# Kernel optimization log

Hardware: AMD Instinct MI355X
Metric: run time of the kernel (lower is better)

Reference implementation:

```python
import jax, jax.numpy as jnp
import numpy as np

B, H, L, D = 4, 16, 2048, 64
TOPK = 128


def setup_inputs() -> dict:
    key = jax.random.key(0)
    k1, k2, k3 = jax.random.split(key, 3)
    Q = jax.random.normal(k1, (B, H, L, D), dtype=jnp.float32)
    K = jax.random.normal(k2, (B, H, L, D), dtype=jnp.float32)
    V = jax.random.normal(k3, (B, H, L, D), dtype=jnp.float32)
    return {"Q": Q, "K": K, "V": V, "topk": TOPK}


def reference(Q, K, V, topk):
    # activation = softmax(d**-0.5 * x), as the docstring prescribes for vanilla attention
    scale = Q.shape[-1] ** -0.5
    neg = -jnp.finfo(Q.dtype).max  # max_neg_value, matching torch
    b, h, lq, d = Q.shape
    lk = K.shape[-2]

    # dots: [B,H,Lq,Lk]
    dots = jnp.einsum('bhqd,bhkd->bhqk', Q, K)
    # causal masking (True entries masked)
    causal = jnp.triu(jnp.ones((lq, lk), dtype=bool), 1)
    dots = jnp.where(causal, neg, dots)

    # top-k sparsification along keys
    top_dots, top_inds = jax.lax.top_k(dots, topk)          # [B,H,Lq,k]
    top_attn = jax.nn.softmax(top_dots * scale, axis=-1)    # activation on top values only

    # scatter activated values back into a zeroed [B,H,Lq,Lk] attention matrix
    bi = jnp.arange(b)[:, None, None, None]
    hi = jnp.arange(h)[None, :, None, None]
    qi = jnp.arange(lq)[None, None, :, None]
    attn = jnp.zeros_like(dots).at[bi, hi, qi, top_inds].set(top_attn)

    # out = attn @ V : [B,H,Lq,Dv]
    return jnp.einsum('bhqk,bhkd->bhqd', attn, V)
```

## Files before the change

kernel.cpp:

```cpp
#include <hip/hip_runtime.h>
#include <float.h>
#include <stdint.h>

#define QB        8
#define NTHREADS  512
#define LQ        2048
#define NDIM      64
#define KSEL      128
#define CHK       512
#define SSTR      516
#define LDS_BYTES 28800
#define WS_NEEDED (2u * 8388608u * 2u)

typedef __attribute__((ext_vector_type(8))) short  s8v;
typedef __attribute__((ext_vector_type(4))) float  f32x4;

__device__ __forceinline__ unsigned ordf(float f) {
  unsigned u = __float_as_uint(f);
  return (u & 0x80000000u) ? ~u : (u | 0x80000000u);
}
__device__ __forceinline__ float unordf(unsigned u) {
  unsigned x = (u & 0x80000000u) ? (u & 0x7FFFFFFFu) : ~u;
  return __uint_as_float(x);
}
__device__ __forceinline__ unsigned short f2bf(float f) {
  unsigned u = __float_as_uint(f);
  return (unsigned short)((u + 0x7FFFu + ((u >> 16) & 1u)) >> 16);
}
__device__ __forceinline__ float bf2f(unsigned short h) {
  return __uint_as_float(((unsigned)h) << 16);
}

extern "C" __global__ void __launch_bounds__(256)
convert_k(const float4* __restrict__ K4, ushort4* __restrict__ Khi,
          ushort4* __restrict__ Klo) {
  const int idx = blockIdx.x * 256 + threadIdx.x;
  const float4 f = K4[idx];
  ushort4 h, l;
  h.x = f2bf(f.x); l.x = f2bf(f.x - bf2f(h.x));
  h.y = f2bf(f.y); l.y = f2bf(f.y - bf2f(h.y));
  h.z = f2bf(f.z); l.z = f2bf(f.z - bf2f(h.z));
  h.w = f2bf(f.w); l.w = f2bf(f.w - bf2f(h.w));
  Khi[idx] = h;
  Klo[idx] = l;
}

__device__ __forceinline__ void select_pv(
    uint4 U0, uint4 U1, uint4 U2, uint4 U3,
    uint4 U4, uint4 U5, uint4 U6, uint4 U7,
    const int g8, const int lane,
    int* __restrict__ list, float* __restrict__ wl,
    const float* __restrict__ Vg, float* __restrict__ outp) {
  const float C = 0.18033688011112042f;
  const unsigned long long ltmask = (1ull << lane) - 1ull;

  unsigned p = 0;
  int k = KSEL;
  bool exact = false;
#pragma unroll 1
  for (int b = 31; b >= 0; --b) {
    const unsigned T = p | (1u << b);
    int cnt = 0;
#define CNT_G(i, Uv) \
    if (i <= g8) { \
      cnt += (int)__popcll(__ballot(Uv.x >= T)); \
      cnt += (int)__popcll(__ballot(Uv.y >= T)); \
      cnt += (int)__popcll(__ballot(Uv.z >= T)); \
      cnt += (int)__popcll(__ballot(Uv.w >= T)); \
    }
    CNT_G(0, U0) CNT_G(1, U1) CNT_G(2, U2) CNT_G(3, U3)
    CNT_G(4, U4) CNT_G(5, U5) CNT_G(6, U6) CNT_G(7, U7)
#undef CNT_G
    if (cnt >= KSEL) {
      p = T;
      if (cnt == KSEL) { exact = true; break; }
    } else {
      k = KSEL - cnt;
    }
  }
  const unsigned tu   = exact ? (p - 1u) : p;
  const int      krem = exact ? 0 : k;
  const float    wt   = exact ? 0.f : exp2f(unordf(p) * C);

  float zacc = 0.f;
  int base = 0;
#define COLL_C(i, uexpr, cidx) { \
    const unsigned ui = (uexpr); \
    const unsigned long long bm = __ballot(ui > tu); \
    if (ui > tu) { \
      const int pos = base + (int)__popcll(bm & ltmask); \
      const float wv = exp2f(unordf(ui) * C); \
      list[pos] = (i << 8) + (lane << 2) + cidx; \
      wl[pos]   = wv; \
      zacc += wv; \
    } \
    base += (int)__popcll(bm); }
#define COLL_G(i, Uv) \
    if (i <= g8) { COLL_C(i, Uv.x, 0) COLL_C(i, Uv.y, 1) COLL_C(i, Uv.z, 2) COLL_C(i, Uv.w, 3) }
  COLL_G(0, U0) COLL_G(1, U1) COLL_G(2, U2) COLL_G(3, U3)
  COLL_G(4, U4) COLL_G(5, U5) COLL_G(6, U6) COLL_G(7, U7)
#undef COLL_G
#undef COLL_C

  int n = base;
  if (wt > 0.f && krem > 0) {
    int carry = 0;
#define TIE_G(i, Uv) \
    if (i <= g8 && carry < krem) { \
      const bool e0 = (Uv.x == tu), e1 = (Uv.y == tu), e2 = (Uv.z == tu), e3 = (Uv.w == tu); \
      const unsigned long long b0 = __ballot(e0), b1 = __ballot(e1); \
      const unsigned long long b2 = __ballot(e2), b3 = __ballot(e3); \
      int r = carry + (int)__popcll(b0 & ltmask) + (int)__popcll(b1 & ltmask) + \
              (int)__popcll(b2 & ltmask) + (int)__popcll(b3 & ltmask); \
      const int jb = (i << 8) + (lane << 2); \
      if (e0) { if (r < krem) { list[base + r] = jb + 0; wl[base + r] = wt; zacc += wt; } ++r; } \
      if (e1) { if (r < krem) { list[base + r] = jb + 1; wl[base + r] = wt; zacc += wt; } ++r; } \
      if (e2) { if (r < krem) { list[base + r] = jb + 2; wl[base + r] = wt; zacc += wt; } ++r; } \
      if (e3) { if (r < krem) { list[base + r] = jb + 3; wl[base + r] = wt; zacc += wt; } ++r; } \
      carry += (int)__popcll(b0) + (int)__popcll(b1) + \
               (int)__popcll(b2) + (int)__popcll(b3); \
    }
    TIE_G(0, U0) TIE_G(1, U1) TIE_G(2, U2) TIE_G(3, U3)
    TIE_G(4, U4) TIE_G(5, U5) TIE_G(6, U6) TIE_G(7, U7)
#undef TIE_G
    n = base + krem;
  }
  float Z = zacc;
#pragma unroll
  for (int off = 1; off < 64; off <<= 1) Z += __shfl_xor(Z, off, 64);
  __threadfence_block();

  const int grp = lane >> 4;
  const int dl4 = (lane & 15) << 2;
  float4 acc4 = {0.f, 0.f, 0.f, 0.f};
  int i = 0;
  for (; i + 8 <= n; i += 8) {
    const int   ja = list[i + grp];
    const int   jb = list[i + 4 + grp];
    const float wa = wl[i + grp];
    const float wb = wl[i + 4 + grp];
    const float4 va = *(const float4*)&Vg[(size_t)ja * NDIM + dl4];
    const float4 vb = *(const float4*)&Vg[(size_t)jb * NDIM + dl4];
    acc4.x += wa * va.x + wb * vb.x;
    acc4.y += wa * va.y + wb * vb.y;
    acc4.z += wa * va.z + wb * vb.z;
    acc4.w += wa * va.w + wb * vb.w;
  }
  for (; i < n; i += 4) {
    const bool  ok = (i + grp) < n;
    const int   j  = ok ? list[i + grp] : 0;
    const float w  = ok ? wl[i + grp]   : 0.f;
    const float4 v = *(const float4*)&Vg[(size_t)j * NDIM + dl4];
    acc4.x += w * v.x;
    acc4.y += w * v.y;
    acc4.z += w * v.z;
    acc4.w += w * v.w;
  }
  acc4.x += __shfl_xor(acc4.x, 16, 64);
  acc4.y += __shfl_xor(acc4.y, 16, 64);
  acc4.z += __shfl_xor(acc4.z, 16, 64);
  acc4.w += __shfl_xor(acc4.w, 16, 64);
  acc4.x += __shfl_xor(acc4.x, 32, 64);
  acc4.y += __shfl_xor(acc4.y, 32, 64);
  acc4.z += __shfl_xor(acc4.z, 32, 64);
  acc4.w += __shfl_xor(acc4.w, 32, 64);
  if (grp == 0) {
    const float rz = 1.f / Z;
    float4 o;
    o.x = acc4.x * rz;
    o.y = acc4.y * rz;
    o.z = acc4.z * rz;
    o.w = acc4.w * rz;
    *(float4*)(outp + dl4) = o;
  }
}

extern "C" __global__ void __launch_bounds__(NTHREADS, 4)
topk_attn_mfma(const float* __restrict__ Qg_, const float* __restrict__ Vg_,
               const unsigned short* __restrict__ Khi_,
               const unsigned short* __restrict__ Klo_,
               float* __restrict__ Out) {
  extern __shared__ char lds[];
  float*          s_chunk = (float*)(lds);
  unsigned short* qs_hi   = (unsigned short*)(lds + 16512);
  unsigned short* qs_lo   = (unsigned short*)(lds + 18560);
  int*            lists   = (int*)(lds + 20608);
  float*          wlist   = (float*)(lds + 24704);

  const int id  = blockIdx.x;
  const int xcd = id & 7;
  const int k   = id >> 3;
  const int bh  = xcd + ((k >> 8) << 3);
  const int qb  = k & 255;

  const int q0   = qb * QB;
  const int tid  = threadIdx.x;
  const int lane = tid & 63;
  const int wid  = tid >> 6;
  const int m16  = lane & 15;
  const int quad = lane >> 4;

  const float* Qg  = Qg_ + ((size_t)(bh * LQ + q0)) * NDIM;
  const float* Vg  = Vg_ + ((size_t)bh) * LQ * NDIM;
  const unsigned short* Khi = Khi_ + ((size_t)bh) * LQ * NDIM;
  const unsigned short* Klo = Klo_ + ((size_t)bh) * LQ * NDIM;

#pragma unroll
  for (int e = tid; e < 16 * NDIM; e += NTHREADS) {
    const int r = e >> 6;
    const float f = (r < QB) ? Qg[e] : 0.f;
    const unsigned short hh = f2bf(f);
    qs_hi[e] = hh;
    qs_lo[e] = f2bf(f - bf2f(hh));
  }
  __syncthreads();

  const unsigned short* qh = qs_hi + m16 * NDIM + quad * 8;
  const unsigned short* ql = qs_lo + m16 * NDIM + quad * 8;
  const s8v Ah0 = *(const s8v*)qh;
  const s8v Ah1 = *(const s8v*)(qh + 32);
  const s8v Al0 = *(const s8v*)ql;
  const s8v Al1 = *(const s8v*)(ql + 32);

  const int q    = q0 + wid;
  const int g8   = q >> 8;
  const int qmax = q0 + QB - 1;
  const int nt   = (qmax >> 4) + 1;
  const int nch  = (qmax >> 9) + 1;

  auto produce = [&](const int ch) {
#pragma unroll 1
    for (int t = 0; t < 4; ++t) {
      const int jt = (ch << 5) + wid + (t << 3);
      if (jt >= nt) continue;
      const int jc  = (jt << 4) + m16;
      const int jcl = jc - (ch << 9);
      const unsigned short* kh = Khi + (size_t)jc * NDIM + quad * 8;
      const unsigned short* kl = Klo + (size_t)jc * NDIM + quad * 8;
      const s8v Bh0 = *(const s8v*)kh;
      const s8v Bh1 = *(const s8v*)(kh + 32);
      const s8v Bl0 = *(const s8v*)kl;
      const s8v Bl1 = *(const s8v*)(kl + 32);
      f32x4 c = {0.f, 0.f, 0.f, 0.f};
      c = __builtin_amdgcn_mfma_f32_16x16x32_bf16(Ah0, Bh0, c, 0, 0, 0);
      c = __builtin_amdgcn_mfma_f32_16x16x32_bf16(Al0, Bh0, c, 0, 0, 0);
      c = __builtin_amdgcn_mfma_f32_16x16x32_bf16(Ah1, Bh1, c, 0, 0, 0);
      c = __builtin_amdgcn_mfma_f32_16x16x32_bf16(Al1, Bh1, c, 0, 0, 0);
      c = __builtin_amdgcn_mfma_f32_16x16x32_bf16(Ah0, Bl0, c, 0, 0, 0);
      c = __builtin_amdgcn_mfma_f32_16x16x32_bf16(Ah1, Bl1, c, 0, 0, 0);
      if (quad < 2) {
#pragma unroll
        for (int reg = 0; reg < 4; ++reg) {
          const int r = quad * 4 + reg;
          s_chunk[r * SSTR + jcl] = c[reg];
        }
      }
    }
  };

  uint4 U0 = make_uint4(0,0,0,0), U1 = make_uint4(0,0,0,0);
  uint4 U2 = make_uint4(0,0,0,0), U3 = make_uint4(0,0,0,0);
  uint4 U4 = make_uint4(0,0,0,0), U5 = make_uint4(0,0,0,0);
  uint4 U6 = make_uint4(0,0,0,0), U7 = make_uint4(0,0,0,0);

  const float4* row4 = (const float4*)(s_chunk + wid * SSTR);
#define CONSUME_HALF(i8, Uv) \
    if (i8 <= g8) { \
      const float4 a = row4[((i8 & 1) << 6) + lane]; \
      const int jb = (i8 << 8) + (lane << 2); \
      Uv.x = (jb + 0 <= q) ? ordf(a.x) : 0u; \
      Uv.y = (jb + 1 <= q) ? ordf(a.y) : 0u; \
      Uv.z = (jb + 2 <= q) ? ordf(a.z) : 0u; \
      Uv.w = (jb + 3 <= q) ? ordf(a.w) : 0u; \
    }

  produce(0);
  __syncthreads();
  CONSUME_HALF(0, U0)
  CONSUME_HALF(1, U1)
  if (nch > 1) {
    __syncthreads();
    produce(1);
    __syncthreads();
    CONSUME_HALF(2, U2)
    CONSUME_HALF(3, U3)
    if (nch > 2) {
      __syncthreads();
      produce(2);
      __syncthreads();
      CONSUME_HALF(4, U4)
      CONSUME_HALF(5, U5)
      if (nch > 3) {
        __syncthreads();
        produce(3);
        __syncthreads();
        CONSUME_HALF(6, U6)
        CONSUME_HALF(7, U7)
      }
    }
  }
#undef CONSUME_HALF

  select_pv(U0, U1, U2, U3, U4, U5, U6, U7, g8, lane,
            lists + wid * KSEL, wlist + wid * KSEL, Vg,
            Out + ((size_t)(bh * LQ + q)) * NDIM);
}

#define FB_QB        8
#define FB_LDS_BYTES 73760

extern "C" __global__ void __launch_bounds__(NTHREADS, 4)
topk_attn_fb(const float* __restrict__ Qg_, const float* __restrict__ Kg_,
             const float* __restrict__ Vg_, float* __restrict__ Out) {
  extern __shared__ char lds[];
  float* s_phys = (float*)(lds);
  int*   lists  = (int*)(lds + 65536);
  float* wlist  = (float*)(lds + 69632);
  float* qs     = (float*)(lds + 65536);

  const int id  = blockIdx.x;
  const int xcd = id & 7;
  const int w   = id >> 3;
  const int bh  = w >> 5;
  const int qb  = ((w & 31) << 3) + xcd;

  const int q0   = qb * FB_QB;
  const int tid  = threadIdx.x;
  const int lane = tid & 63;
  const int wid  = tid >> 6;

  const float* Qg = Qg_ + ((size_t)(bh * LQ + q0)) * NDIM;
  const float* Kg = Kg_ + ((size_t)bh) * LQ * NDIM;
  const float* Vg = Vg_ + ((size_t)bh) * LQ * NDIM;

  if (tid < FB_QB * NDIM / 4) ((float4*)qs)[tid] = ((const float4*)Qg)[tid];
  __syncthreads();

  const int tq   = tid >> 8;
  const int tk   = tid & 255;
  const int j0   = tk << 3;
  const int qmax = q0 + FB_QB - 1;
  const bool active = (j0 <= qmax);

  float acc[4][8];
#pragma unroll
  for (int i = 0; i < 4; ++i)
#pragma unroll
    for (int j = 0; j < 8; ++j) acc[i][j] = 0.f;

  if (active) {
    const float4* K4  = (const float4*)(Kg + (size_t)j0 * NDIM);
    const float4* qs4 = (const float4*)(qs + tq * 4 * NDIM);
#pragma unroll 1
    for (int d4 = 0; d4 < 16; ++d4) {
      float4 qv[4];
#pragma unroll
      for (int i = 0; i < 4; ++i) qv[i] = qs4[i * 16 + d4];
#pragma unroll
      for (int g = 0; g < 4; ++g) {
        const float4 k0 = K4[(2 * g + 0) * 16 + d4];
        const float4 k1 = K4[(2 * g + 1) * 16 + d4];
#pragma unroll
        for (int i = 0; i < 4; ++i) {
          acc[i][2 * g + 0] += qv[i].x * k0.x + qv[i].y * k0.y +
                               qv[i].z * k0.z + qv[i].w * k0.w;
          acc[i][2 * g + 1] += qv[i].x * k1.x + qv[i].y * k1.y +
                               qv[i].z * k1.z + qv[i].w * k1.w;
        }
      }
    }
  }
  __syncthreads();

#pragma unroll
  for (int i = 0; i < 4; ++i) {
    const int q = q0 + tq * 4 + i;
    float4* srow4 = (float4*)(s_phys + (tq * 4 + i) * LQ);
    float4 lo, hi;
    lo.x = (j0 + 0 <= q) ? acc[i][0] : -FLT_MAX;
    lo.y = (j0 + 1 <= q) ? acc[i][1] : -FLT_MAX;
    lo.z = (j0 + 2 <= q) ? acc[i][2] : -FLT_MAX;
    lo.w = (j0 + 3 <= q) ? acc[i][3] : -FLT_MAX;
    hi.x = (j0 + 4 <= q) ? acc[i][4] : -FLT_MAX;
    hi.y = (j0 + 5 <= q) ? acc[i][5] : -FLT_MAX;
    hi.z = (j0 + 6 <= q) ? acc[i][6] : -FLT_MAX;
    hi.w = (j0 + 7 <= q) ? acc[i][7] : -FLT_MAX;
    srow4[tk * 2 + 0] = lo;
    srow4[tk * 2 + 1] = hi;
  }
  __syncthreads();

  const float C = 0.18033688011112042f;
  const int qi = wid;
  const int q = q0 + qi;
  const float* srow = s_phys + qi * LQ;
  const float4* srow4 = (const float4*)srow;

  unsigned u[32];
#pragma unroll
  for (int i = 0; i < 8; ++i) {
    const float4 v = srow4[lane + (i << 6)];
    u[4 * i + 0] = ordf(v.x);
    u[4 * i + 1] = ordf(v.y);
    u[4 * i + 2] = ordf(v.z);
    u[4 * i + 3] = ordf(v.w);
  }

  unsigned p = 0;
  int k = KSEL;
#pragma unroll 1
  for (int b = 31; b >= 0; --b) {
    const unsigned T = p | (1u << b);
    int cnt = 0;
#pragma unroll
    for (int i = 0; i < 32; ++i)
      cnt += (int)__popcll(__ballot(u[i] >= T));
    if (cnt >= KSEL) p = T;
    else             k = KSEL - cnt;
  }
  const unsigned tu = p;
  const int krem = k;
  const float wt = exp2f(unordf(tu) * C);

  const unsigned long long ltmask = (1ull << lane) - 1ull;
  float zacc = 0.f;
  int myeq = 0;
  int base = 0;
#pragma unroll
  for (int i = 0; i < 32; ++i) {
    const unsigned ui = u[i];
    const unsigned long long b = __ballot(ui > tu);
    if (ui > tu) {
      const int pos = base + (int)__popcll(b & ltmask);
      const int j = ((i >> 2) << 8) + (lane << 2) + (i & 3);
      const float wv = exp2f(unordf(ui) * C);
      lists[qi * KSEL + pos] = j;
      wlist[qi * KSEL + pos] = wv;
      zacc += wv;
    }
    base += (int)__popcll(b);
    myeq += (ui == tu) ? 1 : 0;
  }
  int n = base;
  if (wt > 0.f) {
    int te = myeq;
#pragma unroll
    for (int off = 1; off < 64; off <<= 1) te += __shfl_xor(te, off, 64);
    if (te == krem) {
#pragma unroll
      for (int i = 0; i < 32; ++i) {
        const unsigned long long b = __ballot(u[i] == tu);
        if (u[i] == tu) {
          const int pos = base + (int)__popcll(b & ltmask);
          const int j = ((i >> 2) << 8) + (lane << 2) + (i & 3);
          lists[qi * KSEL + pos] = j;
          wlist[qi * KSEL + pos] = wt;
          zacc += wt;
        }
        base += (int)__popcll(b);
      }
      n = base;
    } else {
      if (lane == 0) {
        int taken = 0, pos = base;
        for (int j = 0; j < LQ && taken < krem; ++j) {
          if (ordf(srow[j]) == tu) {
            lists[qi * KSEL + pos] = j;
            wlist[qi * KSEL + pos] = wt;
            pos++; taken++;
          }
        }
        zacc += wt * (float)krem;
      }
      n = KSEL;
    }
  }
  float Z = zacc;
#pragma unroll
  for (int off = 1; off < 64; off <<= 1) Z += __shfl_xor(Z, off, 64);
  __threadfence_block();

  float accv = 0.f;
  int i = 0;
  for (; i + 8 <= n; i += 8) {
    const int4   ja = *(const int4*)  &lists[qi * KSEL + i];
    const int4   jb = *(const int4*)  &lists[qi * KSEL + i + 4];
    const float4 wa = *(const float4*)&wlist[qi * KSEL + i];
    const float4 wb = *(const float4*)&wlist[qi * KSEL + i + 4];
    const float v0 = Vg[(size_t)ja.x * NDIM + lane];
    const float v1 = Vg[(size_t)ja.y * NDIM + lane];
    const float v2 = Vg[(size_t)ja.z * NDIM + lane];
    const float v3 = Vg[(size_t)ja.w * NDIM + lane];
    const float v4 = Vg[(size_t)jb.x * NDIM + lane];
    const float v5 = Vg[(size_t)jb.y * NDIM + lane];
    const float v6 = Vg[(size_t)jb.z * NDIM + lane];
    const float v7 = Vg[(size_t)jb.w * NDIM + lane];
    accv += wa.x * v0 + wa.y * v1 + wa.z * v2 + wa.w * v3 +
            wb.x * v4 + wb.y * v5 + wb.z * v6 + wb.w * v7;
  }
  for (; i < n; ++i) {
    const int j = lists[qi * KSEL + i];
    accv += wlist[qi * KSEL + i] * Vg[(size_t)j * NDIM + lane];
  }
  Out[((size_t)(bh * LQ + q)) * NDIM + lane] = accv / Z;
}

extern "C" void kernel_launch(void* const* d_in, const int* in_sizes, int n_in,
                              void* d_out, int out_size, void* d_ws, size_t ws_size,
                              hipStream_t stream) {
  (void)in_sizes; (void)n_in; (void)out_size;
  const float* Q = (const float*)d_in[0];
  const float* K = (const float*)d_in[1];
  const float* V = (const float*)d_in[2];
  float* Out = (float*)d_out;

  if (ws_size >= WS_NEEDED) {
    ushort4* Khi = (ushort4*)d_ws;
    ushort4* Klo = (ushort4*)((char*)d_ws + 8388608u * 2u);
    convert_k<<<dim3(8192), 256, 0, stream>>>((const float4*)K, Khi, Klo);

    (void)hipFuncSetAttribute(reinterpret_cast<const void*>(&topk_attn_mfma),
                              hipFuncAttributeMaxDynamicSharedMemorySize, LDS_BYTES);
    topk_attn_mfma<<<dim3(16384), NTHREADS, LDS_BYTES, stream>>>(
        Q, V, (const unsigned short*)Khi, (const unsigned short*)Klo, Out);
  } else {
    (void)hipFuncSetAttribute(reinterpret_cast<const void*>(&topk_attn_fb),
                              hipFuncAttributeMaxDynamicSharedMemorySize, FB_LDS_BYTES);
    topk_attn_fb<<<dim3(16384), NTHREADS, FB_LDS_BYTES, stream>>>(Q, K, V, Out);
  }
}
```

Baseline: 870.7 us.

## Process 16 query rows per block so each wave selects two rows

Each block now covers 16 queries instead of 8, filling the full 16-row MFMA tile that was previously half padding, so every K tile loaded feeds twice as many useful rows. Each wave holds two rows' score registers and runs the radix top-k threshold search for both rows interleaved in one loop, then collects and multiplies by V for each. The grid is halved. In exchange, LDS use and register pressure roughly double per block, which may lower occupancy and lengthen the serial select phase per wave.

Measured after the change: 850.0 us. -2.4%, faster.

```diff
diff --git a/kernel.cpp b/kernel.cpp
--- a/kernel.cpp
+++ b/kernel.cpp
@@ -2,14 +2,14 @@
 #include <float.h>
 #include <stdint.h>
 
-#define QB        8
+#define QB        16
 #define NTHREADS  512
 #define LQ        2048
 #define NDIM      64
 #define KSEL      128
 #define CHK       512
 #define SSTR      516
-#define LDS_BYTES 28800
+#define LDS_BYTES 53504
 #define WS_NEEDED (2u * 8388608u * 2u)
 
 typedef __attribute__((ext_vector_type(8))) short  s8v;
@@ -45,41 +45,18 @@
   Klo[idx] = l;
 }
 
-__device__ __forceinline__ void select_pv(
+__device__ __forceinline__ void collect_pv(
     uint4 U0, uint4 U1, uint4 U2, uint4 U3,
     uint4 U4, uint4 U5, uint4 U6, uint4 U7,
+    const unsigned p, const int kr, const bool exact,
     const int g8, const int lane,
     int* __restrict__ list, float* __restrict__ wl,
     const float* __restrict__ Vg, float* __restrict__ outp) {
   const float C = 0.18033688011112042f;
   const unsigned long long ltmask = (1ull << lane) - 1ull;
 
-  unsigned p = 0;
-  int k = KSEL;
-  bool exact = false;
-#pragma unroll 1
-  for (int b = 31; b >= 0; --b) {
-    const unsigned T = p | (1u << b);
-    int cnt = 0;
-#define CNT_G(i, Uv) \
-    if (i <= g8) { \
-      cnt += (int)__popcll(__ballot(Uv.x >= T)); \
-      cnt += (int)__popcll(__ballot(Uv.y >= T)); \
-      cnt += (int)__popcll(__ballot(Uv.z >= T)); \
-      cnt += (int)__popcll(__ballot(Uv.w >= T)); \
-    }
-    CNT_G(0, U0) CNT_G(1, U1) CNT_G(2, U2) CNT_G(3, U3)
-    CNT_G(4, U4) CNT_G(5, U5) CNT_G(6, U6) CNT_G(7, U7)
-#undef CNT_G
-    if (cnt >= KSEL) {
-      p = T;
-      if (cnt == KSEL) { exact = true; break; }
-    } else {
-      k = KSEL - cnt;
-    }
-  }
   const unsigned tu   = exact ? (p - 1u) : p;
-  const int      krem = exact ? 0 : k;
+  const int      krem = exact ? 0 : kr;
   const float    wt   = exact ? 0.f : exp2f(unordf(p) * C);
 
   float zacc = 0.f;
@@ -182,16 +159,16 @@
                float* __restrict__ Out) {
   extern __shared__ char lds[];
   float*          s_chunk = (float*)(lds);
-  unsigned short* qs_hi   = (unsigned short*)(lds + 16512);
-  unsigned short* qs_lo   = (unsigned short*)(lds + 18560);
-  int*            lists   = (int*)(lds + 20608);
-  float*          wlist   = (float*)(lds + 24704);
+  unsigned short* qs_hi   = (unsigned short*)(lds + 33024);
+  unsigned short* qs_lo   = (unsigned short*)(lds + 35072);
+  int*            lists   = (int*)(lds + 37120);
+  float*          wlist   = (float*)(lds + 45312);
 
   const int id  = blockIdx.x;
   const int xcd = id & 7;
   const int k   = id >> 3;
-  const int bh  = xcd + ((k >> 8) << 3);
-  const int qb  = k & 255;
+  const int bh  = xcd + ((k >> 7) << 3);
+  const int qb  = k & 127;
 
   const int q0   = qb * QB;
   const int tid  = threadIdx.x;
@@ -206,9 +183,8 @@
   const unsigned short* Klo = Klo_ + ((size_t)bh) * LQ * NDIM;
 
 #pragma unroll
-  for (int e = tid; e < 16 * NDIM; e += NTHREADS) {
-    const int r = e >> 6;
-    const float f = (r < QB) ? Qg[e] : 0.f;
+  for (int e = tid; e < QB * NDIM; e += NTHREADS) {
+    const float f = Qg[e];
     const unsigned short hh = f2bf(f);
     qs_hi[e] = hh;
     qs_lo[e] = f2bf(f - bf2f(hh));
@@ -222,8 +198,9 @@
   const s8v Al0 = *(const s8v*)ql;
   const s8v Al1 = *(const s8v*)(ql + 32);
 
-  const int q    = q0 + wid;
-  const int g8   = q >> 8;
+  const int qa   = q0 + wid;
+  const int qbq  = q0 + wid + 8;
+  const int g8   = qa >> 8;
   const int qmax = q0 + QB - 1;
   const int nt   = (qmax >> 4) + 1;
   const int nch  = (qmax >> 9) + 1;
@@ -248,12 +225,9 @@
       c = __builtin_amdgcn_mfma_f32_16x16x32_bf16(Al1, Bh1, c, 0, 0, 0);
       c = __builtin_amdgcn_mfma_f32_16x16x32_bf16(Ah0, Bl0, c, 0, 0, 0);
       c = __builtin_amdgcn_mfma_f32_16x16x32_bf16(Ah1, Bl1, c, 0, 0, 0);
-      if (quad < 2) {
-#pragma unroll
-        for (int reg = 0; reg < 4; ++reg) {
-          const int r = quad * 4 + reg;
-          s_chunk[r * SSTR + jcl] = c[reg];
-        }
+#pragma unroll
+      for (int reg = 0; reg < 4; ++reg) {
+        s_chunk[(quad * 4 + reg) * SSTR + jcl] = c[reg];
       }
     }
   };
@@ -262,48 +236,98 @@
   uint4 U2 = make_uint4(0,0,0,0), U3 = make_uint4(0,0,0,0);
   uint4 U4 = make_uint4(0,0,0,0), U5 = make_uint4(0,0,0,0);
   uint4 U6 = make_uint4(0,0,0,0), U7 = make_uint4(0,0,0,0);
-
-  const float4* row4 = (const float4*)(s_chunk + wid * SSTR);
-#define CONSUME_HALF(i8, Uv) \
+  uint4 W0 = make_uint4(0,0,0,0), W1 = make_uint4(0,0,0,0);
+  uint4 W2 = make_uint4(0,0,0,0), W3 = make_uint4(0,0,0,0);
+  uint4 W4 = make_uint4(0,0,0,0), W5 = make_uint4(0,0,0,0);
+  uint4 W6 = make_uint4(0,0,0,0), W7 = make_uint4(0,0,0,0);
+
+  const float4* rowA = (const float4*)(s_chunk + wid * SSTR);
+  const float4* rowB = (const float4*)(s_chunk + (wid + 8) * SSTR);
+#define CONSUME_HALF(i8, Uv, Wv) \
     if (i8 <= g8) { \
-      const float4 a = row4[((i8 & 1) << 6) + lane]; \
+      const float4 a = rowA[((i8 & 1) << 6) + lane]; \
+      const float4 bb = rowB[((i8 & 1) << 6) + lane]; \
       const int jb = (i8 << 8) + (lane << 2); \
-      Uv.x = (jb + 0 <= q) ? ordf(a.x) : 0u; \
-      Uv.y = (jb + 1 <= q) ? ordf(a.y) : 0u; \
-      Uv.z = (jb + 2 <= q) ? ordf(a.z) : 0u; \
-      Uv.w = (jb + 3 <= q) ? ordf(a.w) : 0u; \
+      Uv.x = (jb + 0 <= qa) ? ordf(a.x) : 0u; \
+      Uv.y = (jb + 1 <= qa) ? ordf(a.y) : 0u; \
+      Uv.z = (jb + 2 <= qa) ? ordf(a.z) : 0u; \
+      Uv.w = (jb + 3 <= qa) ? ordf(a.w) : 0u; \
+      Wv.x = (jb + 0 <= qbq) ? ordf(bb.x) : 0u; \
+      Wv.y = (jb + 1 <= qbq) ? ordf(bb.y) : 0u; \
+      Wv.z = (jb + 2 <= qbq) ? ordf(bb.z) : 0u; \
+      Wv.w = (jb + 3 <= qbq) ? ordf(bb.w) : 0u; \
     }
 
   produce(0);
   __syncthreads();
-  CONSUME_HALF(0, U0)
-  CONSUME_HALF(1, U1)
+  CONSUME_HALF(0, U0, W0)
+  CONSUME_HALF(1, U1, W1)
   if (nch > 1) {
     __syncthreads();
     produce(1);
     __syncthreads();
-    CONSUME_HALF(2, U2)
-    CONSUME_HALF(3, U3)
+    CONSUME_HALF(2, U2, W2)
+    CONSUME_HALF(3, U3, W3)
     if (nch > 2) {
       __syncthreads();
       produce(2);
       __syncthreads();
-      CONSUME_HALF(4, U4)
-      CONSUME_HALF(5, U5)
+      CONSUME_HALF(4, U4, W4)
+      CONSUME_HALF(5, U5, W5)
       if (nch > 3) {
         __syncthreads();
         produce(3);
         __syncthreads();
-        CONSUME_HALF(6, U6)
-        CONSUME_HALF(7, U7)
+        CONSUME_HALF(6, U6, W6)
+        CONSUME_HALF(7, U7, W7)
       }
     }
   }
 #undef CONSUME_HALF
 
-  select_pv(U0, U1, U2, U3, U4, U5, U6, U7, g8, lane,
-            lists + wid * KSEL, wlist + wid * KSEL, Vg,
-            Out + ((size_t)(bh * LQ + q)) * NDIM);
+  unsigned pa = 0, pb = 0;
+  int ka = KSEL, kb = KSEL;
+  bool ea = false, eb = false;
+#define CNT_ONE(i, Uv, T, cnt) \
+    if (i <= g8) { \
+      cnt += (int)__popcll(__ballot(Uv.x >= T)); \
+      cnt += (int)__popcll(__ballot(Uv.y >= T)); \
+      cnt += (int)__popcll(__ballot(Uv.z >= T)); \
+      cnt += (int)__popcll(__ballot(Uv.w >= T)); \
+    }
+#pragma unroll 1
+  for (int b = 31; b >= 0; --b) {
+    const unsigned bit = 1u << b;
+    if (!ea) {
+      const unsigned T = pa | bit;
+      int cnt = 0;
+      CNT_ONE(0, U0, T, cnt) CNT_ONE(1, U1, T, cnt)
+      CNT_ONE(2, U2, T, cnt) CNT_ONE(3, U3, T, cnt)
+      CNT_ONE(4, U4, T, cnt) CNT_ONE(5, U5, T, cnt)
+      CNT_ONE(6, U6, T, cnt) CNT_ONE(7, U7, T, cnt)
+      if (cnt >= KSEL) { pa = T; if (cnt == KSEL) ea = true; }
+      else             ka = KSEL - cnt;
+    }
+    if (!eb) {
+      const unsigned T = pb | bit;
+      int cnt = 0;
+      CNT_ONE(0, W0, T, cnt) CNT_ONE(1, W1, T, cnt)
+      CNT_ONE(2, W2, T, cnt) CNT_ONE(3, W3, T, cnt)
+      CNT_ONE(4, W4, T, cnt) CNT_ONE(5, W5, T, cnt)
+      CNT_ONE(6, W6, T, cnt) CNT_ONE(7, W7, T, cnt)
+      if (cnt >= KSEL) { pb = T; if (cnt == KSEL) eb = true; }
+      else             kb = KSEL - cnt;
+    }
+    if (ea && eb) break;
+  }
+#undef CNT_ONE
+
+  collect_pv(U0, U1, U2, U3, U4, U5, U6, U7, pa, ka, ea, g8, lane,
+             lists + wid * KSEL, wlist + wid * KSEL, Vg,
+             Out + ((size_t)(bh * LQ + qa)) * NDIM);
+  collect_pv(W0, W1, W2, W3, W4, W5, W6, W7, pb, kb, eb, g8, lane,
+             lists + (wid + 8) * KSEL, wlist + (wid + 8) * KSEL, Vg,
+             Out + ((size_t)(bh * LQ + qbq)) * NDIM);
 }
 
 #define FB_QB        8
@@ -521,7 +545,7 @@
 
     (void)hipFuncSetAttribute(reinterpret_cast<const void*>(&topk_attn_mfma),
                               hipFuncAttributeMaxDynamicSharedMemorySize, LDS_BYTES);
-    topk_attn_mfma<<<dim3(16384), NTHREADS, LDS_BYTES, stream>>>(
+    topk_attn_mfma<<<dim3(8192), NTHREADS, LDS_BYTES, stream>>>(
         Q, V, (const unsigned short*)Khi, (const unsigned short*)Klo, Out);
   } else {
     (void)hipFuncSetAttribute(reinterpret_cast<const void*>(&topk_attn_fb),
```
